# Kernel optimization log

Hardware: AMD Instinct MI355X
Metric: run time of the kernel (lower is better)

## Reference

```python
import jax, jax.numpy as jnp
import numpy as np

D_MODEL = 1024
NUM_HEADS = 16


def setup_inputs() -> dict:
    key = jax.random.key(0)
    ks = jax.random.split(key, 5)
    B, S, D = 2, 2048, D_MODEL
    x = jax.random.normal(ks[0], (B, S, D), dtype=jnp.float32)
    # nn.Linear(d_model, d_model, bias=False) weights, shape [out, in]
    scale = 1.0 / np.sqrt(D)
    Wq = jax.random.normal(ks[1], (D, D), dtype=jnp.float32) * scale
    Wk = jax.random.normal(ks[2], (D, D), dtype=jnp.float32) * scale
    Wv = jax.random.normal(ks[3], (D, D), dtype=jnp.float32) * scale
    Wo = jax.random.normal(ks[4], (D, D), dtype=jnp.float32) * scale
    return {"x": x, "Wq": Wq, "Wk": Wk, "Wv": Wv, "Wo": Wo}


def reference(x, Wq, Wk, Wv, Wo):
    B, S, D = x.shape
    H = NUM_HEADS
    dh = D // H
    # projections: x @ W.T (Linear without bias)
    q = (x @ Wq.T).reshape(B, S, H, dh).transpose(0, 2, 1, 3)  # [B,H,S,dh]
    k = (x @ Wk.T).reshape(B, S, H, dh).transpose(0, 2, 1, 3)
    v = (x @ Wv.T).reshape(B, S, H, dh).transpose(0, 2, 1, 3)
    scores = jnp.einsum("bhqd,bhkd->bhqk", q, k) / jnp.sqrt(jnp.float32(dh))
    # causal mask: positions j > i get -inf before softmax
    causal = jnp.triu(jnp.ones((S, S), dtype=bool), k=1)
    scores = jnp.where(causal, -jnp.inf, scores)
    attn = jax.nn.softmax(scores, axis=-1)  # [B,H,S,S]
    out = jnp.einsum("bhqk,bhkd->bhqd", attn, v)  # [B,H,S,dh]
    out = out.transpose(0, 2, 1, 3).reshape(B, S, D)
    return out @ Wo.T
```

## Files before the change

kernel.cpp:

```cpp
#include <hip/hip_runtime.h>

typedef __attribute__((ext_vector_type(8))) __bf16 bf16x8;
typedef __attribute__((ext_vector_type(4))) __bf16 bf16x4;
typedef __attribute__((ext_vector_type(2))) __bf16 bf16x2;
typedef __attribute__((ext_vector_type(4))) float f32x4;
typedef __attribute__((ext_vector_type(16))) float f32x16;
typedef __attribute__((ext_vector_type(4))) unsigned uint4v;

static constexpr int S = 2048;
static constexpr int D = 1024;
static constexpr int BATCH = 2;
static constexpr int M_ROWS = BATCH * S;

#define GLOAD_LDS16(gp, lp)                                                        \
  __builtin_amdgcn_global_load_lds((const __attribute__((address_space(1))) void*)(gp), \
                                   (__attribute__((address_space(3))) void*)(lp), 16, 0, 0)

__global__ __launch_bounds__(256) void cast_f32_bf16(const float* __restrict__ in,
                                                     __bf16* __restrict__ out) {
  int i = (blockIdx.x * 256 + threadIdx.x) * 4;
  *reinterpret_cast<bf16x4*>(out + i) =
      __builtin_convertvector(*reinterpret_cast<const f32x4*>(in + i), bf16x4);
}

__global__ __launch_bounds__(256) void cast_w4(const float* __restrict__ w0, const float* __restrict__ w1,
                                               const float* __restrict__ w2, const float* __restrict__ w3,
                                               __bf16* __restrict__ o0, __bf16* __restrict__ o1,
                                               __bf16* __restrict__ o2, __bf16* __restrict__ o3) {
  const float* in = blockIdx.y == 0 ? w0 : blockIdx.y == 1 ? w1 : blockIdx.y == 2 ? w2 : w3;
  __bf16* out = blockIdx.y == 0 ? o0 : blockIdx.y == 1 ? o1 : blockIdx.y == 2 ? o2 : o3;
  int i = (blockIdx.x * 256 + threadIdx.x) * 4;
  *reinterpret_cast<bf16x4*>(out + i) =
      __builtin_convertvector(*reinterpret_cast<const f32x4*>(in + i), bf16x4);
}

template <typename OutT>
__device__ __forceinline__ void gemm_core(const __bf16* __restrict__ A,
                                          const __bf16* __restrict__ Bm,
                                          OutT* __restrict__ C, int m0, int n0, int K, int ldc,
                                          __bf16* At, __bf16* Bt) {
  const int tid = threadIdx.x;
  const int w = tid >> 6, l = tid & 63;
  const int wr = w >> 1, wc = w & 1;
  const int ln = l & 15, gr = l >> 4;

  const int srow = w * 32 + (l >> 2);
  const int scol = (l & 3) * 8;
  const size_t aoff = (size_t)(m0 + srow) * K + scol;
  const size_t boff = (size_t)(n0 + srow) * K + scol;
  __bf16* lA = At + w * 2 * 512;
  __bf16* lB = Bt + w * 2 * 512;

  f32x4 acc[4][4] = {};

  for (int k0 = 0; k0 < K; k0 += 32) {
    __syncthreads();
    GLOAD_LDS16(A + aoff + k0, lA);
    GLOAD_LDS16(A + aoff + (size_t)16 * K + k0, lA + 512);
    GLOAD_LDS16(Bm + boff + k0, lB);
    GLOAD_LDS16(Bm + boff + (size_t)16 * K + k0, lB + 512);
    __syncthreads();

    bf16x8 af[4], bfr[4];
#pragma unroll
    for (int mi = 0; mi < 4; mi++)
      af[mi] = *reinterpret_cast<const bf16x8*>(&At[(wr * 64 + mi * 16 + ln) * 32 + gr * 8]);
#pragma unroll
    for (int ni = 0; ni < 4; ni++)
      bfr[ni] = *reinterpret_cast<const bf16x8*>(&Bt[(wc * 64 + ni * 16 + ln) * 32 + gr * 8]);
#pragma unroll
    for (int mi = 0; mi < 4; mi++)
#pragma unroll
      for (int ni = 0; ni < 4; ni++)
        acc[mi][ni] = __builtin_amdgcn_mfma_f32_16x16x32_bf16(af[mi], bfr[ni], acc[mi][ni], 0, 0, 0);
  }

#pragma unroll
  for (int mi = 0; mi < 4; mi++)
#pragma unroll
    for (int ni = 0; ni < 4; ni++)
#pragma unroll
      for (int r = 0; r < 4; r++) {
        int row = m0 + wr * 64 + mi * 16 + gr * 4 + r;
        int col = n0 + wc * 64 + ni * 16 + ln;
        float v = acc[mi][ni][r];
        if constexpr (__is_same(OutT, float))
          C[(size_t)row * ldc + col] = v;
        else
          C[(size_t)row * ldc + col] = (__bf16)v;
      }
}

__global__ __launch_bounds__(256) void qkv_gemm(const __bf16* __restrict__ xb,
                                                const __bf16* __restrict__ wq,
                                                const __bf16* __restrict__ wk,
                                                const __bf16* __restrict__ wv,
                                                __bf16* __restrict__ q, __bf16* __restrict__ k,
                                                __bf16* __restrict__ vt) {
  __shared__ __bf16 At[128 * 32];
  __shared__ __bf16 Bt[128 * 32];
  const int id = blockIdx.x;
  const __bf16 *A, *B;
  __bf16* C;
  int m0, n0, ldc;
  if (id < 512) {
    A = xb;
    B = (id < 256) ? wq : wk;
    C = (id < 256) ? q : k;
    int t = id & 255;
    m0 = (t >> 3) * 128;
    n0 = (t & 7) * 128;
    ldc = 1024;
  } else {
    int t = id - 512;
    A = wv;
    B = xb;
    C = vt;
    m0 = (t & 7) * 128;
    n0 = (t >> 3) * 128;
    ldc = 4096;
  }
  gemm_core<__bf16>(A, B, C, m0, n0, 1024, ldc, At, Bt);
}

__global__ __launch_bounds__(256) void wo_gemm(const __bf16* __restrict__ ob,
                                               const __bf16* __restrict__ wo,
                                               float* __restrict__ out) {
  __shared__ __bf16 At[128 * 32];
  __shared__ __bf16 Bt[128 * 32];
  gemm_core<float>(ob, wo, out, blockIdx.y * 128, blockIdx.x * 128, 1024, 1024, At, Bt);
}

__global__ __launch_bounds__(512, 2) void attn_kernel(const __bf16* __restrict__ Qb,
                                                      const __bf16* __restrict__ Kb,
                                                      const __bf16* __restrict__ VTb,
                                                      __bf16* __restrict__ Ob) {
  const int lin = blockIdx.x;
  const int wid = ((lin & 7) << 5) | (lin >> 3);
  const int bh = wid >> 3;
  const int j = wid & 7;
  const int b = bh >> 4, h = bh & 15;

  const int tid = threadIdx.x;
  const int w = tid >> 6, l = tid & 63;
  const int q31 = l & 31, hi = l >> 5;

  int qt;
  switch (w) {
    case 0: qt = j; break;
    case 1: qt = 16 + j; break;
    case 2: qt = 15 - j; break;
    case 3: qt = 31 - j; break;
    case 4: qt = 63 - j; break;
    case 5: qt = 47 - j; break;
    case 6: qt = 48 + j; break;
    default: qt = 32 + j; break;
  }
  const int q0 = qt * 32;
  const int n = qt + 1;
  const int na = (n + 1) >> 1;
  const int nb = n >> 1;

  const __bf16* Qp = Qb + (size_t)b * S * D + h * 64;
  const __bf16* Kp = Kb + (size_t)b * S * D + h * 64;
  const __bf16* Vt = VTb + (size_t)(h * 64) * M_ROWS + b * S;

  const float SCALE2 = 0.125f * 1.44269504f;
  const float NEG = -1e30f;
  const float THR_RAW = 8.0f / SCALE2;

  bf16x8 qf[4];
#pragma unroll
  for (int ds = 0; ds < 4; ds++)
    qf[ds] = *reinterpret_cast<const bf16x8*>(
        Qp + (size_t)(q0 + q31) * D + ds * 16 + hi * 8);

  f32x16 oaccA[2] = {}, oaccB[2] = {};
  float mrA = NEG, lsA = 0.f, mrB = NEG, lsB = 0.f;

  auto loadK = [&](bf16x8 (&dst)[4], int kk) {
#pragma unroll
    for (int ds = 0; ds < 4; ds++)
      dst[ds] = *reinterpret_cast<const bf16x8*>(
          Kp + (size_t)(kk + q31) * D + ds * 16 + hi * 8);
  };
  auto loadV = [&](bf16x8 (&dst)[2][2], int kk) {
#pragma unroll
    for (int d0 = 0; d0 < 2; d0++)
#pragma unroll
      for (int ks = 0; ks < 2; ks++)
        dst[d0][ks] = *reinterpret_cast<const bf16x8*>(
            Vt + (size_t)(d0 * 32 + q31) * M_ROWS + kk + ks * 16 + hi * 8);
  };
  auto qk1 = [&](f32x16& st, bf16x8 (&kf)[4]) {
    f32x16 z = {};
#pragma unroll
    for (int ds = 0; ds < 4; ds++)
      z = __builtin_amdgcn_mfma_f32_32x32x16_bf16(kf[ds], qf[ds], z, 0, 0, 0);
    st = z;
  };
  auto pack2 = [](float x, float y) -> unsigned {
    bf16x2 p;
    p[0] = (__bf16)x;
    p[1] = (__bf16)y;
    return __builtin_bit_cast(unsigned, p);
  };
  auto maskmax = [&](f32x16& st, bool tail, float (&pv)[16]) -> float {
#pragma unroll
    for (int r = 0; r < 16; r++) {
      float v = st[r];
      if (tail) {
        int keyidx = (r & 3) + 8 * (r >> 2) + 4 * hi;
        v = (keyidx <= q31) ? v : NEG;
      }
      pv[r] = v;
    }
    float t8[8], t4[4];
#pragma unroll
    for (int ii = 0; ii < 8; ii++) t8[ii] = fmaxf(pv[ii], pv[ii + 8]);
#pragma unroll
    for (int ii = 0; ii < 4; ii++) t4[ii] = fmaxf(t8[ii], t8[ii + 4]);
    float tm = fmaxf(fmaxf(t4[0], t4[1]), fmaxf(t4[2], t4[3]));
    return fmaxf(tm, __shfl_xor(tm, 32));
  };
  auto rescale = [&](float& mr, float& ls, f32x16& o0, f32x16& o1, float tm) {
    float nm = fmaxf(mr, tm);
    float a = __builtin_exp2f((mr - nm) * SCALE2);
    mr = nm;
    ls *= a;
#pragma unroll
    for (int r = 0; r < 16; r++) o0[r] *= a;
#pragma unroll
    for (int r = 0; r < 16; r++) o1[r] *= a;
  };
  auto expsum = [&](float (&pv)[16], float mr, float& ls, unsigned (&dw)[8]) {
    const float mrs = mr * SCALE2;
#pragma unroll
    for (int r = 0; r < 16; r++)
      pv[r] = __builtin_exp2f(__builtin_fmaf(pv[r], SCALE2, -mrs));
    float s8[8], s4[4];
#pragma unroll
    for (int ii = 0; ii < 8; ii++) s8[ii] = pv[ii] + pv[ii + 8];
#pragma unroll
    for (int ii = 0; ii < 4; ii++) s4[ii] = s8[ii] + s8[ii + 4];
    float ps = (s4[0] + s4[1]) + (s4[2] + s4[3]);
    ps += __shfl_xor(ps, 32);
    ls += ps;
#pragma unroll
    for (int bb = 0; bb < 4; bb++) {
      dw[2 * bb] = pack2(pv[4 * bb], pv[4 * bb + 1]);
      dw[2 * bb + 1] = pack2(pv[4 * bb + 2], pv[4 * bb + 3]);
    }
  };
  auto pvmma = [&](unsigned (&dw)[8], bf16x8 (&vf)[2][2], f32x16& o0, f32x16& o1) {
#pragma unroll
    for (int ks = 0; ks < 2; ks++) {
      unsigned s0v = hi ? dw[4 * ks + 0] : dw[4 * ks + 2];
      unsigned s1v = hi ? dw[4 * ks + 1] : dw[4 * ks + 3];
      unsigned r0 = (unsigned)__shfl_xor((int)s0v, 32);
      unsigned r1 = (unsigned)__shfl_xor((int)s1v, 32);
      uint4v uv;
      uv.x = hi ? r0 : dw[4 * ks + 0];
      uv.y = hi ? r1 : dw[4 * ks + 1];
      uv.z = hi ? dw[4 * ks + 2] : r0;
      uv.w = hi ? dw[4 * ks + 3] : r1;
      bf16x8 pb = __builtin_bit_cast(bf16x8, uv);
      o0 = __builtin_amdgcn_mfma_f32_32x32x16_bf16(vf[0][ks], pb, o0, 0, 0, 0);
      o1 = __builtin_amdgcn_mfma_f32_32x32x16_bf16(vf[1][ks], pb, o1, 0, 0, 0);
    }
  };

  bf16x8 kfA[4], kfB[4], vfA[2][2], vfB[2][2];
  f32x16 stA, stB;

  loadK(kfA, 0);
  if (nb > 0) loadK(kfB, na * 32);

  for (int i = 0; i < nb; i++) {
    loadV(vfA, i * 32);
    loadV(vfB, (na + i) * 32);
    __builtin_amdgcn_s_setprio(1);
    qk1(stA, kfA);
    qk1(stB, kfB);
    __builtin_amdgcn_s_setprio(0);
    if (i + 1 < na) loadK(kfA, (i + 1) * 32);
    if (i + 1 < nb) loadK(kfB, (na + i + 1) * 32);

    float pvA[16], pvB[16];
    float tmA = maskmax(stA, false, pvA);
    float tmB = maskmax(stB, i == nb - 1, pvB);
    if (!__all((tmA - mrA <= THR_RAW) && (tmB - mrB <= THR_RAW))) {
      rescale(mrA, lsA, oaccA[0], oaccA[1], tmA);
      rescale(mrB, lsB, oaccB[0], oaccB[1], tmB);
    }
    unsigned dwA[8], dwB[8];
    expsum(pvA, mrA, lsA, dwA);
    expsum(pvB, mrB, lsB, dwB);
    __builtin_amdgcn_s_setprio(1);
    pvmma(dwA, vfA, oaccA[0], oaccA[1]);
    pvmma(dwB, vfB, oaccB[0], oaccB[1]);
    __builtin_amdgcn_s_setprio(0);
  }
  if (na > nb) {
    const int i = na - 1;
    loadV(vfA, i * 32);
    __builtin_amdgcn_s_setprio(1);
    qk1(stA, kfA);
    __builtin_amdgcn_s_setprio(0);
    float pvA[16];
    float tmA = maskmax(stA, n == 1, pvA);
    if (!__all(tmA - mrA <= THR_RAW)) rescale(mrA, lsA, oaccA[0], oaccA[1], tmA);
    unsigned dwA[8];
    expsum(pvA, mrA, lsA, dwA);
    __builtin_amdgcn_s_setprio(1);
    pvmma(dwA, vfA, oaccA[0], oaccA[1]);
    __builtin_amdgcn_s_setprio(0);
  }

  {
    float mc = fmaxf(mrA, mrB);
    float a0 = __builtin_exp2f((mrA - mc) * SCALE2);
    float a1 = __builtin_exp2f((mrB - mc) * SCALE2);
    float inv = 1.0f / (lsA * a0 + lsB * a1);
    float f0 = a0 * inv, f1 = a1 * inv;
    size_t row = (size_t)(b * S + q0 + q31);
#pragma unroll
    for (int d0 = 0; d0 < 2; d0++)
#pragma unroll
      for (int bb = 0; bb < 4; bb++) {
        bf16x4 ov;
#pragma unroll
        for (int rr = 0; rr < 4; rr++)
          ov[rr] = (__bf16)(oaccA[d0][4 * bb + rr] * f0 + oaccB[d0][4 * bb + rr] * f1);
        *reinterpret_cast<bf16x4*>(Ob + row * D + h * 64 + d0 * 32 + 8 * bb + 4 * hi) = ov;
      }
  }
}

extern "C" void kernel_launch(void* const* d_in, const int* in_sizes, int n_in,
                              void* d_out, int out_size, void* d_ws, size_t ws_size,
                              hipStream_t stream) {
  const float* x = (const float*)d_in[0];
  const float* Wq = (const float*)d_in[1];
  const float* Wk = (const float*)d_in[2];
  const float* Wv = (const float*)d_in[3];
  const float* Wo = (const float*)d_in[4];
  float* out = (float*)d_out;

  char* ws = (char*)d_ws;
  const size_t MB = 1024 * 1024;
  __bf16* xb = (__bf16*)(ws + 0 * MB);
  __bf16* qb = (__bf16*)(ws + 8 * MB);
  __bf16* kb = (__bf16*)(ws + 16 * MB);
  __bf16* vtb = (__bf16*)(ws + 24 * MB);
  __bf16* ob = (__bf16*)(ws + 32 * MB);
  __bf16* wqb = (__bf16*)(ws + 40 * MB);
  __bf16* wkb = (__bf16*)(ws + 42 * MB);
  __bf16* wvb = (__bf16*)(ws + 44 * MB);
  __bf16* wob = (__bf16*)(ws + 46 * MB);

  const int nx = M_ROWS * D;
  const int nw = D * D;

  cast_f32_bf16<<<nx / 4 / 256, 256, 0, stream>>>(x, xb);
  cast_w4<<<dim3(nw / 4 / 256, 4), 256, 0, stream>>>(Wq, Wk, Wv, Wo, wqb, wkb, wvb, wob);

  qkv_gemm<<<768, 256, 0, stream>>>(xb, wqb, wkb, wvb, qb, kb, vtb);

  attn_kernel<<<256, 512, 0, stream>>>(qb, kb, vtb, ob);

  wo_gemm<<<dim3(8, 32), 256, 0, stream>>>(ob, wob, out);
}
```

Baseline: 142.4 us.

## Pair complementary query tiles per wave and split key ranges across wave halves

Each wave now handles two query tiles, j and 63-j, so the causal work per wave is balanced. The key range of each tile is split between two waves (hf=0/1), and their partial softmax states are merged through shared memory. V loads are also moved to prefetch the next iteration. The cost is extra LDS use, a block-wide barrier and bf16 rounding of the partial accumulators, which may cost some accuracy and occupancy.

```diff
diff --git a/kernel.cpp b/kernel.cpp
--- a/kernel.cpp
+++ b/kernel.cpp
@@ -135,31 +135,26 @@
                                                       const __bf16* __restrict__ Kb,
                                                       const __bf16* __restrict__ VTb,
                                                       __bf16* __restrict__ Ob) {
+  __shared__ __bf16 mo[8][64][32];
+  __shared__ float mml[8][64][2];
+
   const int lin = blockIdx.x;
   const int wid = ((lin & 7) << 5) | (lin >> 3);
   const int bh = wid >> 3;
-  const int j = wid & 7;
+  const int ib = wid & 7;
   const int b = bh >> 4, h = bh & 15;
 
   const int tid = threadIdx.x;
   const int w = tid >> 6, l = tid & 63;
   const int q31 = l & 31, hi = l >> 5;
-
-  int qt;
-  switch (w) {
-    case 0: qt = j; break;
-    case 1: qt = 16 + j; break;
-    case 2: qt = 15 - j; break;
-    case 3: qt = 31 - j; break;
-    case 4: qt = 63 - j; break;
-    case 5: qt = 47 - j; break;
-    case 6: qt = 48 + j; break;
-    default: qt = 32 + j; break;
-  }
-  const int q0 = qt * 32;
-  const int n = qt + 1;
-  const int na = (n + 1) >> 1;
-  const int nb = n >> 1;
+  const int pp = w & 3, hf = w >> 2;
+
+  const int j = ib * 4 + pp;
+  const int q0A = j * 32, q0B = (63 - j) * 32;
+  const int nA = j + 1, nB = 64 - j;
+  const int nhA = (nA + 1) >> 1, nhB = (nB + 1) >> 1;
+  const int sA = hf ? nhA : 0, cA = hf ? nA - nhA : nhA;
+  const int sB = hf ? nhB : 0, cB = hf ? nB - nhB : nhB;
 
   const __bf16* Qp = Qb + (size_t)b * S * D + h * 64;
   const __bf16* Kp = Kb + (size_t)b * S * D + h * 64;
@@ -169,11 +164,12 @@
   const float NEG = -1e30f;
   const float THR_RAW = 8.0f / SCALE2;
 
-  bf16x8 qf[4];
-#pragma unroll
-  for (int ds = 0; ds < 4; ds++)
-    qf[ds] = *reinterpret_cast<const bf16x8*>(
-        Qp + (size_t)(q0 + q31) * D + ds * 16 + hi * 8);
+  bf16x8 qfA[4], qfB[4];
+#pragma unroll
+  for (int ds = 0; ds < 4; ds++) {
+    qfA[ds] = *reinterpret_cast<const bf16x8*>(Qp + (size_t)(q0A + q31) * D + ds * 16 + hi * 8);
+    qfB[ds] = *reinterpret_cast<const bf16x8*>(Qp + (size_t)(q0B + q31) * D + ds * 16 + hi * 8);
+  }
 
   f32x16 oaccA[2] = {}, oaccB[2] = {};
   float mrA = NEG, lsA = 0.f, mrB = NEG, lsB = 0.f;
@@ -192,7 +188,7 @@
         dst[d0][ks] = *reinterpret_cast<const bf16x8*>(
             Vt + (size_t)(d0 * 32 + q31) * M_ROWS + kk + ks * 16 + hi * 8);
   };
-  auto qk1 = [&](f32x16& st, bf16x8 (&kf)[4]) {
+  auto qk1 = [&](f32x16& st, bf16x8 (&kf)[4], bf16x8 (&qf)[4]) {
     f32x16 z = {};
 #pragma unroll
     for (int ds = 0; ds < 4; ds++)
@@ -273,22 +269,24 @@
   bf16x8 kfA[4], kfB[4], vfA[2][2], vfB[2][2];
   f32x16 stA, stB;
 
-  loadK(kfA, 0);
-  if (nb > 0) loadK(kfB, na * 32);
-
-  for (int i = 0; i < nb; i++) {
-    loadV(vfA, i * 32);
-    loadV(vfB, (na + i) * 32);
+  if (cA > 0) {
+    loadK(kfA, sA * 32);
+    loadV(vfA, sA * 32);
+  }
+  loadK(kfB, sB * 32);
+  loadV(vfB, sB * 32);
+
+  for (int i2 = 0; i2 < cA; i2++) {
     __builtin_amdgcn_s_setprio(1);
-    qk1(stA, kfA);
-    qk1(stB, kfB);
+    qk1(stA, kfA, qfA);
+    qk1(stB, kfB, qfB);
     __builtin_amdgcn_s_setprio(0);
-    if (i + 1 < na) loadK(kfA, (i + 1) * 32);
-    if (i + 1 < nb) loadK(kfB, (na + i + 1) * 32);
+    if (i2 + 1 < cA) loadK(kfA, (sA + i2 + 1) * 32);
+    if (i2 + 1 < cB) loadK(kfB, (sB + i2 + 1) * 32);
 
     float pvA[16], pvB[16];
-    float tmA = maskmax(stA, false, pvA);
-    float tmB = maskmax(stB, i == nb - 1, pvB);
+    float tmA = maskmax(stA, sA + i2 == nA - 1, pvA);
+    float tmB = maskmax(stB, sB + i2 == nB - 1, pvB);
     if (!__all((tmA - mrA <= THR_RAW) && (tmB - mrB <= THR_RAW))) {
       rescale(mrA, lsA, oaccA[0], oaccA[1], tmA);
       rescale(mrB, lsB, oaccB[0], oaccB[1], tmB);
@@ -300,40 +298,79 @@
     pvmma(dwA, vfA, oaccA[0], oaccA[1]);
     pvmma(dwB, vfB, oaccB[0], oaccB[1]);
     __builtin_amdgcn_s_setprio(0);
-  }
-  if (na > nb) {
-    const int i = na - 1;
-    loadV(vfA, i * 32);
+    if (i2 + 1 < cA) loadV(vfA, (sA + i2 + 1) * 32);
+    if (i2 + 1 < cB) loadV(vfB, (sB + i2 + 1) * 32);
+  }
+  for (int i2 = cA; i2 < cB; i2++) {
     __builtin_amdgcn_s_setprio(1);
-    qk1(stA, kfA);
+    qk1(stB, kfB, qfB);
     __builtin_amdgcn_s_setprio(0);
-    float pvA[16];
-    float tmA = maskmax(stA, n == 1, pvA);
-    if (!__all(tmA - mrA <= THR_RAW)) rescale(mrA, lsA, oaccA[0], oaccA[1], tmA);
-    unsigned dwA[8];
-    expsum(pvA, mrA, lsA, dwA);
+    if (i2 + 1 < cB) loadK(kfB, (sB + i2 + 1) * 32);
+    float pvB[16];
+    float tmB = maskmax(stB, sB + i2 == nB - 1, pvB);
+    if (!__all(tmB - mrB <= THR_RAW)) rescale(mrB, lsB, oaccB[0], oaccB[1], tmB);
+    unsigned dwB[8];
+    expsum(pvB, mrB, lsB, dwB);
     __builtin_amdgcn_s_setprio(1);
-    pvmma(dwA, vfA, oaccA[0], oaccA[1]);
+    pvmma(dwB, vfB, oaccB[0], oaccB[1]);
     __builtin_amdgcn_s_setprio(0);
-  }
-
-  {
-    float mc = fmaxf(mrA, mrB);
-    float a0 = __builtin_exp2f((mrA - mc) * SCALE2);
-    float a1 = __builtin_exp2f((mrB - mc) * SCALE2);
-    float inv = 1.0f / (lsA * a0 + lsB * a1);
-    float f0 = a0 * inv, f1 = a1 * inv;
-    size_t row = (size_t)(b * S + q0 + q31);
-#pragma unroll
-    for (int d0 = 0; d0 < 2; d0++)
-#pragma unroll
-      for (int bb = 0; bb < 4; bb++) {
-        bf16x4 ov;
-#pragma unroll
-        for (int rr = 0; rr < 4; rr++)
-          ov[rr] = (__bf16)(oaccA[d0][4 * bb + rr] * f0 + oaccB[d0][4 * bb + rr] * f1);
-        *reinterpret_cast<bf16x4*>(Ob + row * D + h * 64 + d0 * 32 + 8 * bb + 4 * hi) = ov;
+    if (i2 + 1 < cB) loadV(vfB, (sB + i2 + 1) * 32);
+  }
+
+  if (hf == 1) {
+#pragma unroll
+    for (int d0 = 0; d0 < 2; d0++) {
+      bf16x8 pkA, pkB;
+#pragma unroll
+      for (int rr = 0; rr < 8; rr++) {
+        pkA[rr] = (__bf16)oaccA[d0][rr];
+        pkB[rr] = (__bf16)oaccB[d0][rr];
       }
+      *reinterpret_cast<bf16x8*>(&mo[2 * pp + 0][l][d0 * 16]) = pkA;
+      *reinterpret_cast<bf16x8*>(&mo[2 * pp + 1][l][d0 * 16]) = pkB;
+      bf16x8 pkA2, pkB2;
+#pragma unroll
+      for (int rr = 0; rr < 8; rr++) {
+        pkA2[rr] = (__bf16)oaccA[d0][8 + rr];
+        pkB2[rr] = (__bf16)oaccB[d0][8 + rr];
+      }
+      *reinterpret_cast<bf16x8*>(&mo[2 * pp + 0][l][d0 * 16 + 8]) = pkA2;
+      *reinterpret_cast<bf16x8*>(&mo[2 * pp + 1][l][d0 * 16 + 8]) = pkB2;
+    }
+    mml[2 * pp + 0][l][0] = mrA;
+    mml[2 * pp + 0][l][1] = lsA;
+    mml[2 * pp + 1][l][0] = mrB;
+    mml[2 * pp + 1][l][1] = lsB;
+  }
+  __syncthreads();
+  if (hf == 0) {
+#pragma unroll
+    for (int cc = 0; cc < 2; cc++) {
+      const int slot = 2 * pp + cc;
+      const int q0 = cc ? q0B : q0A;
+      f32x16* oacc = cc ? oaccB : oaccA;
+      float mr = cc ? mrB : mrA;
+      float ls = cc ? lsB : lsA;
+      float mr1 = mml[slot][l][0], ls1 = mml[slot][l][1];
+      float mc = fmaxf(mr, mr1);
+      float a0 = __builtin_exp2f((mr - mc) * SCALE2);
+      float a1 = __builtin_exp2f((mr1 - mc) * SCALE2);
+      float inv = 1.0f / (ls * a0 + ls1 * a1);
+      float f0 = a0 * inv, f1 = a1 * inv;
+      size_t row = (size_t)(b * S + q0 + q31);
+#pragma unroll
+      for (int d0 = 0; d0 < 2; d0++)
+#pragma unroll
+        for (int bb = 0; bb < 4; bb++) {
+          bf16x4 ov;
+#pragma unroll
+          for (int rr = 0; rr < 4; rr++) {
+            float part = (float)mo[slot][l][d0 * 16 + 4 * bb + rr];
+            ov[rr] = (__bf16)(oacc[d0][4 * bb + rr] * f0 + part * f1);
+          }
+          *reinterpret_cast<bf16x4*>(Ob + row * D + h * 64 + d0 * 32 + 8 * bb + 4 * hi) = ov;
+        }
+    }
   }
 }
 
```

Measured after the change: 141.7 us. About the same (-0.5%).
